# Kernel optimization log

Measured on AMD Instinct MI355X. Metric: run time of the kernel, lower is better.

The kernel has to match this reference:

```python
import jax, jax.numpy as jnp
import numpy as np

B, T, C, H, E, K = 4, 2048, 1024, 2048, 8, 2


def setup_inputs() -> dict:
    key = jax.random.key(0)
    ks = jax.random.split(key, 9)
    s = lambda k, shape, fan: jax.random.normal(k, shape, jnp.float32) / np.sqrt(fan)
    return {
        "x": jax.random.normal(ks[0], (B, T, C), jnp.float32),
        "gate_w": s(ks[1], (C, E), C),            # router gate (no bias)
        "sg_w": s(ks[2], (C, H), C),              # shared expert: gate proj
        "su_w": s(ks[3], (C, H), C),              # shared expert: up proj
        "sd_w": s(ks[4], (H, C), H),              # shared expert: down proj
        "eg_w": s(ks[5], (E, C, H), C),           # routed experts: gate proj
        "eu_w": s(ks[6], (E, C, H), C),           # routed experts: up proj
        "ed_w": s(ks[7], (E, H, C), H),           # routed experts: down proj
    }


def _swiglu(x, wg, wu, wd):
    # x: (B,T,C) -> (B,T,C)
    return jnp.einsum("bth,hc->btc", jax.nn.silu(jnp.einsum("btc,ch->bth", x, wg)) * jnp.einsum("btc,ch->bth", x, wu), wd)


def reference(x, gate_w, sg_w, su_w, sd_w, eg_w, eu_w, ed_w):
    # Router: top-k over expert logits, softmax over selected logits
    logits = jnp.einsum("btc,ce->bte", x, gate_w)            # (B,T,E)
    topk_logits, topk_idx = jax.lax.top_k(logits, K)         # (B,T,K)
    weights = jax.nn.softmax(topk_logits, axis=-1)           # (B,T,K)
    # Dense per-expert combine weight: w_e[b,t,e] = sum_k weights*(idx==e)
    onehot = jax.nn.one_hot(topk_idx, E, dtype=x.dtype)      # (B,T,K,E)
    dense_w = jnp.einsum("btk,btke->bte", weights, onehot)   # (B,T,E)

    shared_out = _swiglu(x, sg_w, su_w, sd_w)

    # Scan over experts (small fixed E), accumulating weighted expert outputs.
    dense_w_e = jnp.moveaxis(dense_w, -1, 0)                 # (E,B,T)

    def step(acc, params):
        wg, wu, wd, w = params
        return acc + w[..., None] * _swiglu(x, wg, wu, wd), None

    expert_out, _ = jax.lax.scan(step, jnp.zeros_like(x), (eg_w, eu_w, ed_w, dense_w_e))
    return shared_out + expert_out, logits
```

## Files before the change

kernel.cpp:

```cpp
#include <hip/hip_runtime.h>
#include <cstdint>
#include <cstddef>

#define NTOK 8192
#define CDIM 1024
#define HDIM 2048
#define NEXP 8
#define NSEG 9
#define MAXTILES 104

typedef __bf16 bf16;
typedef unsigned short u16;
typedef __attribute__((ext_vector_type(8))) __bf16 bf16x8;
typedef __attribute__((ext_vector_type(4))) float f32x4;

__device__ __forceinline__ u16 f2bf(float f) {
  union { u16 u; __bf16 b; } cv;
  cv.b = (__bf16)f;
  return cv.u;
}

__device__ __forceinline__ void gload_lds16(const bf16* g, bf16* l) {
  __builtin_amdgcn_global_load_lds(
      (const __attribute__((address_space(1))) unsigned int*)g,
      (__attribute__((address_space(3))) unsigned int*)l, 16, 0, 0);
}

__global__ __launch_bounds__(64) void init_kernel(int* __restrict__ counts,
                                                  int* __restrict__ fill) {
  if (threadIdx.x < NEXP) {
    counts[threadIdx.x] = 0;
    fill[threadIdx.x] = 0;
  }
}

__global__ __launch_bounds__(256) void cast_x_kernel(
    const float* __restrict__ src, bf16* __restrict__ dst) {
  size_t i = ((size_t)blockIdx.x * 256 + threadIdx.x) * 8;
  float4 a = *(const float4*)(src + i);
  float4 b = *(const float4*)(src + i + 4);
  bf16x8 p;
  p[0] = (bf16)a.x; p[1] = (bf16)a.y; p[2] = (bf16)a.z; p[3] = (bf16)a.w;
  p[4] = (bf16)b.x; p[5] = (bf16)b.y; p[6] = (bf16)b.z; p[7] = (bf16)b.w;
  *(bf16x8*)(dst + i) = p;
}

__global__ __launch_bounds__(256) void router2_kernel(
    const float* __restrict__ x, const float* __restrict__ gw,
    float* __restrict__ logits_out, int* __restrict__ tk_e,
    float* __restrict__ tk_w, int* __restrict__ counts) {
  int wv = threadIdx.x >> 6, l = threadIdx.x & 63;
  int t = blockIdx.x * 4 + wv;
  const float* xr = x + (size_t)t * CDIM;
  float acc[NEXP];
#pragma unroll
  for (int e = 0; e < NEXP; ++e) acc[e] = 0.f;
  for (int c = l; c < CDIM; c += 64) {
    float xv = xr[c];
    const float* g = gw + (size_t)c * NEXP;
    float4 g0 = *(const float4*)(g);
    float4 g1 = *(const float4*)(g + 4);
    acc[0] += xv * g0.x; acc[1] += xv * g0.y; acc[2] += xv * g0.z; acc[3] += xv * g0.w;
    acc[4] += xv * g1.x; acc[5] += xv * g1.y; acc[6] += xv * g1.z; acc[7] += xv * g1.w;
  }
#pragma unroll
  for (int off = 32; off > 0; off >>= 1) {
#pragma unroll
    for (int e = 0; e < NEXP; ++e) acc[e] += __shfl_xor(acc[e], off, 64);
  }
  int e0 = 0; float l0 = acc[0];
#pragma unroll
  for (int e = 1; e < NEXP; ++e) { if (acc[e] > l0) { l0 = acc[e]; e0 = e; } }
  int e1 = -1; float l1 = -3.4e38f;
#pragma unroll
  for (int e = 0; e < NEXP; ++e) { if (e != e0 && acc[e] > l1) { l1 = acc[e]; e1 = e; } }
  float ex = expf(l1 - l0);
  float w0 = 1.f / (1.f + ex), w1 = ex / (1.f + ex);
  if (l < NEXP) logits_out[(size_t)t * NEXP + l] = acc[l];
  if (l == 0) {
    tk_e[2 * t] = e0; tk_e[2 * t + 1] = e1;
    tk_w[2 * t] = w0; tk_w[2 * t + 1] = w1;
    atomicAdd(&counts[e0], 1);
    atomicAdd(&counts[e1], 1);
  }
}

__global__ __launch_bounds__(256) void offsets_kernel(
    const int* __restrict__ counts, int* __restrict__ offs_g,
    int* __restrict__ tile_seg, int* __restrict__ list_tok) {
  __shared__ int off[NSEG], pad[NSEG], cnt[NSEG], ntot;
  int tid = threadIdx.x;
  if (tid == 0) {
    int tot = 0;
    for (int e = 0; e < NSEG; ++e) {
      int c = (e < NEXP) ? counts[e] : NTOK;
      cnt[e] = c; off[e] = tot;
      int p = (c + 255) & ~255;
      pad[e] = p; tot += p;
    }
    ntot = tot;
  }
  __syncthreads();
  if (tid < NSEG) offs_g[tid] = off[tid];
  for (int gt = tid; gt < MAXTILES; gt += 256) {
    int row = gt * 256, seg = -1;
    if (row < ntot) {
      for (int e = 0; e < NSEG; ++e)
        if (row >= off[e] && row < off[e] + pad[e]) { seg = e; break; }
    }
    tile_seg[gt] = seg;
  }
  for (int e = 0; e < NSEG; ++e)
    for (int i = off[e] + cnt[e] + tid; i < off[e] + pad[e]; i += 256)
      list_tok[i] = 0;
}

__global__ __launch_bounds__(256) void scatter_kernel(
    const int* __restrict__ tk_e, const int* __restrict__ offs,
    int* __restrict__ fill, int* __restrict__ list_tok,
    int* __restrict__ inv) {
  int t = blockIdx.x * 256 + threadIdx.x;
  int e0 = tk_e[2 * t], e1 = tk_e[2 * t + 1];
  int p0 = atomicAdd(&fill[e0], 1);
  int i0 = offs[e0] + p0;
  list_tok[i0] = t; inv[2 * t] = i0;
  int p1 = atomicAdd(&fill[e1], 1);
  int i1 = offs[e1] + p1;
  list_tok[i1] = t; inv[2 * t + 1] = i1;
  list_tok[offs[NEXP] + t] = t;
}

__device__ __forceinline__ void transpose_body(const float* __restrict__ src,
                                               u16* __restrict__ dst, int R, int C) {
  __shared__ uint32_t t32[64 * 33];
  const int tid = threadIdx.x;
  const int r0 = blockIdx.y * 64, c0 = blockIdx.x * 64;
  const int rp = tid >> 3;
  const int cg = tid & 7;
  const float* s0 = src + (size_t)(r0 + 2 * rp) * C + c0 + 8 * cg;
  const float* s1 = s0 + C;
  float4 a0 = *(const float4*)(s0);
  float4 a1 = *(const float4*)(s0 + 4);
  float4 b0 = *(const float4*)(s1);
  float4 b1 = *(const float4*)(s1 + 4);
  uint32_t p[8];
  p[0] = f2bf(a0.x) | ((uint32_t)f2bf(b0.x) << 16);
  p[1] = f2bf(a0.y) | ((uint32_t)f2bf(b0.y) << 16);
  p[2] = f2bf(a0.z) | ((uint32_t)f2bf(b0.z) << 16);
  p[3] = f2bf(a0.w) | ((uint32_t)f2bf(b0.w) << 16);
  p[4] = f2bf(a1.x) | ((uint32_t)f2bf(b1.x) << 16);
  p[5] = f2bf(a1.y) | ((uint32_t)f2bf(b1.y) << 16);
  p[6] = f2bf(a1.z) | ((uint32_t)f2bf(b1.z) << 16);
  p[7] = f2bf(a1.w) | ((uint32_t)f2bf(b1.w) << 16);
#pragma unroll
  for (int c = 0; c < 8; ++c) t32[(8 * cg + c) * 33 + rp] = p[c];
  __syncthreads();
  const int oc = tid >> 2, og = tid & 3;
  const uint32_t* rb = &t32[oc * 33 + 8 * og];
  union { uint32_t w[8]; uint4 v[2]; } u;
#pragma unroll
  for (int k = 0; k < 8; ++k) u.w[k] = rb[k];
  u16* d = dst + (size_t)(c0 + oc) * R + r0 + 16 * og;
  *(uint4*)d = u.v[0];
  *(uint4*)(d + 8) = u.v[1];
}

__global__ __launch_bounds__(256) void transpose_cast_kernel(
    const float* __restrict__ src, u16* __restrict__ dst, int R, int C) {
  transpose_body(src, dst, R, C);
}

__global__ __launch_bounds__(256) void transpose_gu_kernel(
    const float* __restrict__ sg, const float* __restrict__ su,
    const float* __restrict__ eg, const float* __restrict__ eu,
    u16* __restrict__ wTg, u16* __restrict__ wTu) {
  const size_t slot = (size_t)HDIM * CDIM;
  int z = blockIdx.z;
  const float* src; u16* dst;
  if (z == 0)       { src = sg;                 dst = wTg + 8 * slot; }
  else if (z == 1)  { src = su;                 dst = wTu + 8 * slot; }
  else if (z < 10)  { src = eg + (z - 2) * slot;  dst = wTg + (z - 2) * slot; }
  else              { src = eu + (z - 10) * slot; dst = wTu + (z - 10) * slot; }
  transpose_body(src, dst, CDIM, HDIM);
}

__global__ __launch_bounds__(256) void transpose_d_kernel(
    const float* __restrict__ sd, const float* __restrict__ ed,
    u16* __restrict__ wTd) {
  const size_t slot = (size_t)HDIM * CDIM;
  int z = blockIdx.z;
  const float* src; u16* dst;
  if (z == 0) { src = sd;                 dst = wTd + 8 * slot; }
  else        { src = ed + (z - 1) * slot; dst = wTd + (z - 1) * slot; }
  transpose_body(src, dst, HDIM, CDIM);
}


#define PHASE_READS_BEGIN __builtin_amdgcn_sched_barrier(0)
#define PHASE_COMPUTE     asm volatile("s_waitcnt lgkmcnt(0)" ::: "memory"); \
                          __builtin_amdgcn_sched_barrier(0);                 \
                          __builtin_amdgcn_s_setprio(1)
#define PHASE_END         __builtin_amdgcn_s_setprio(0)

__global__ __launch_bounds__(512, 2) void gemm_gu5(
    const bf16* __restrict__ xb, const bf16* __restrict__ wTg,
    const bf16* __restrict__ wTu, const int* __restrict__ tile_seg,
    const int* __restrict__ list_tok, bf16* __restrict__ act) {
  __shared__ __align__(16) bf16 sS[2][32768];
  __shared__ int tokLds[256];

  const int nwg = gridDim.x;
  const int bid = blockIdx.x;
  const int wid = (bid & 7) * (nwg >> 3) + (bid >> 3);
  const int tileIdx = wid % MAXTILES;
  const int colIdx = wid / MAXTILES;
  const int seg = tile_seg[tileIdx];
  if (seg < 0) return;

  const int tid = threadIdx.x, l = tid & 63, wv = tid >> 6;
  const int wr = wv >> 2, wn = wv & 3;
  const int n0 = colIdx * 128;
  const size_t rowbase = (size_t)tileIdx * 256;

  if (tid < 256) tokLds[tid] = list_tok[rowbase + tid];
  __syncthreads();

  const int row8 = tid >> 3;
  const int scol = (((tid & 7) ^ (row8 & 7)) << 3);
  const bf16* gA0 = xb + (size_t)tokLds[row8] * CDIM + scol;
  const bf16* gA1 = xb + (size_t)tokLds[64 + row8] * CDIM + scol;
  const bf16* gA2 = xb + (size_t)tokLds[128 + row8] * CDIM + scol;
  const bf16* gA3 = xb + (size_t)tokLds[192 + row8] * CDIM + scol;
  const size_t wslot = (size_t)seg * HDIM * CDIM;
  const bf16* gBg = wTg + wslot + (size_t)(n0 + row8) * CDIM + scol;
  const bf16* gBu = wTu + wslot + (size_t)(n0 + row8) * CDIM + scol;
  const int t8 = tid * 8;

  const int fr = l & 15, kq = l >> 4;
  const int cS0 = ((kq ^ (l & 7)) << 4);
  const int cS1 = (((4 | kq) ^ (l & 7)) << 4);
  const int aBase = (wr * 128 + fr) * 128;
  const int gBase = 32768 + (wn * 32 + fr) * 128;
  const int uBase = 49152 + (wn * 32 + fr) * 128;

  f32x4 accG[2][4][2], accU[2][4][2];
#pragma unroll
  for (int h = 0; h < 2; ++h)
#pragma unroll
    for (int i = 0; i < 4; ++i)
#pragma unroll
      for (int j = 0; j < 2; ++j) {
        accG[h][i][j] = (f32x4){0.f, 0.f, 0.f, 0.f};
        accU[h][i][j] = (f32x4){0.f, 0.f, 0.f, 0.f};
      }

  auto stage_all = [&](int b, int k0) {
    bf16* d = &sS[b][0];
    gload_lds16(gA0 + k0, d + t8);
    gload_lds16(gA1 + k0, d + 4096 + t8);
    gload_lds16(gA2 + k0, d + 8192 + t8);
    gload_lds16(gA3 + k0, d + 12288 + t8);
    gload_lds16(gBg + k0, d + 16384 + t8);
    gload_lds16(gBg + 64 * CDIM + k0, d + 20480 + t8);
    gload_lds16(gBu + k0, d + 24576 + t8);
    gload_lds16(gBu + 64 * CDIM + k0, d + 28672 + t8);
  };

  constexpr int NKT = CDIM / 64;
  stage_all(0, 0);

  for (int kt = 0; kt < NKT; ++kt) {
    const int b = kt & 1, bn = b ^ 1;
    const bool more = (kt + 1 < NKT);
    __builtin_amdgcn_s_barrier();
    if (more) stage_all(bn, (kt + 1) * 64);
    if (more) asm volatile("s_waitcnt vmcnt(8)" ::: "memory");
    else      asm volatile("s_waitcnt vmcnt(0)" ::: "memory");
    __builtin_amdgcn_s_barrier();
    const char* pS = (const char*)&sS[b][0];
    bf16x8 af[4][2], bg[2][2], bu[2][2];

    PHASE_READS_BEGIN;
#pragma unroll
    for (int i = 0; i < 4; ++i) {
      af[i][0] = *(const bf16x8*)(pS + aBase + i * 2048 + cS0);
      af[i][1] = *(const bf16x8*)(pS + aBase + i * 2048 + cS1);
    }
#pragma unroll
    for (int j = 0; j < 2; ++j) {
      bg[j][0] = *(const bf16x8*)(pS + gBase + j * 2048 + cS0);
      bg[j][1] = *(const bf16x8*)(pS + gBase + j * 2048 + cS1);
    }
    PHASE_COMPUTE;
#pragma unroll
    for (int i = 0; i < 4; ++i)
#pragma unroll
      for (int j = 0; j < 2; ++j) {
        accG[0][i][j] = __builtin_amdgcn_mfma_f32_16x16x32_bf16(af[i][0], bg[j][0], accG[0][i][j], 0, 0, 0);
        accG[0][i][j] = __builtin_amdgcn_mfma_f32_16x16x32_bf16(af[i][1], bg[j][1], accG[0][i][j], 0, 0, 0);
      }
    PHASE_END;

    PHASE_READS_BEGIN;
#pragma unroll
    for (int j = 0; j < 2; ++j) {
      bu[j][0] = *(const bf16x8*)(pS + uBase + j * 2048 + cS0);
      bu[j][1] = *(const bf16x8*)(pS + uBase + j * 2048 + cS1);
    }
    PHASE_COMPUTE;
#pragma unroll
    for (int i = 0; i < 4; ++i)
#pragma unroll
      for (int j = 0; j < 2; ++j) {
        accU[0][i][j] = __builtin_amdgcn_mfma_f32_16x16x32_bf16(af[i][0], bu[j][0], accU[0][i][j], 0, 0, 0);
        accU[0][i][j] = __builtin_amdgcn_mfma_f32_16x16x32_bf16(af[i][1], bu[j][1], accU[0][i][j], 0, 0, 0);
      }
    PHASE_END;

    PHASE_READS_BEGIN;
#pragma unroll
    for (int i = 0; i < 4; ++i) {
      af[i][0] = *(const bf16x8*)(pS + aBase + 8192 + i * 2048 + cS0);
      af[i][1] = *(const bf16x8*)(pS + aBase + 8192 + i * 2048 + cS1);
    }
    PHASE_COMPUTE;
#pragma unroll
    for (int i = 0; i < 4; ++i)
#pragma unroll
      for (int j = 0; j < 2; ++j) {
        accG[1][i][j] = __builtin_amdgcn_mfma_f32_16x16x32_bf16(af[i][0], bg[j][0], accG[1][i][j], 0, 0, 0);
        accG[1][i][j] = __builtin_amdgcn_mfma_f32_16x16x32_bf16(af[i][1], bg[j][1], accG[1][i][j], 0, 0, 0);
      }
    PHASE_END;

    __builtin_amdgcn_s_setprio(1);
#pragma unroll
    for (int i = 0; i < 4; ++i)
#pragma unroll
      for (int j = 0; j < 2; ++j) {
        accU[1][i][j] = __builtin_amdgcn_mfma_f32_16x16x32_bf16(af[i][0], bu[j][0], accU[1][i][j], 0, 0, 0);
        accU[1][i][j] = __builtin_amdgcn_mfma_f32_16x16x32_bf16(af[i][1], bu[j][1], accU[1][i][j], 0, 0, 0);
      }
    __builtin_amdgcn_s_setprio(0);
  }

  const int cn = n0 + wn * 32 + fr;
  const int rb = wr * 128 + kq * 4;
#pragma unroll
  for (int h = 0; h < 2; ++h)
#pragma unroll
    for (int i = 0; i < 4; ++i)
#pragma unroll
      for (int r = 0; r < 4; ++r) {
        const size_t row = rowbase + rb + h * 64 + i * 16 + r;
#pragma unroll
        for (int j = 0; j < 2; ++j) {
          float g = accG[h][i][j][r], uu = accU[h][i][j][r];
          float s = g / (1.f + expf(-g));
          act[row * HDIM + cn + j * 16] = (bf16)(s * uu);
        }
      }
}

__global__ __launch_bounds__(512, 2) void gemm_down5(
    const bf16* __restrict__ act, const bf16* __restrict__ wTd,
    const int* __restrict__ tile_seg, bf16* __restrict__ dbuf) {
  __shared__ __align__(16) bf16 sS[2][32768];

  const int nwg = gridDim.x;
  const int bid = blockIdx.x;
  const int wid = (bid & 7) * (nwg >> 3) + (bid >> 3);
  const int tileIdx = wid % MAXTILES;
  const int colIdx = wid / MAXTILES;
  const int seg = tile_seg[tileIdx];
  if (seg < 0) return;

  const int tid = threadIdx.x, l = tid & 63, wv = tid >> 6;
  const int wr = wv >> 2, wn = wv & 3;
  const int n0 = colIdx * 256;
  const size_t rowbase = (size_t)tileIdx * 256;

  const int row8 = tid >> 3;
  const int scol = (((tid & 7) ^ (row8 & 7)) << 3);
  const bf16* gA0 = act + (rowbase + row8) * HDIM + scol;
  const bf16* gA1 = act + (rowbase + 64 + row8) * HDIM + scol;
  const bf16* gA2 = act + (rowbase + 128 + row8) * HDIM + scol;
  const bf16* gA3 = act + (rowbase + 192 + row8) * HDIM + scol;
  const bf16* gB  = wTd + (size_t)seg * CDIM * HDIM + (size_t)(n0 + row8) * HDIM + scol;
  const int t8 = tid * 8;

  const int fr = l & 15, kq = l >> 4;
  const int cS0 = ((kq ^ (l & 7)) << 4);
  const int cS1 = (((4 | kq) ^ (l & 7)) << 4);
  const int aBase = (wr * 128 + fr) * 128;
  const int bBase = 32768 + (wn * 64 + fr) * 128;

  f32x4 acc[2][2][4][2];
#pragma unroll
  for (int h = 0; h < 2; ++h)
#pragma unroll
    for (int nh = 0; nh < 2; ++nh)
#pragma unroll
      for (int i = 0; i < 4; ++i)
#pragma unroll
        for (int j = 0; j < 2; ++j) acc[h][nh][i][j] = (f32x4){0.f, 0.f, 0.f, 0.f};

  auto stage_all = [&](int b, int k0) {
    bf16* d = &sS[b][0];
    gload_lds16(gA0 + k0, d + t8);
    gload_lds16(gA1 + k0, d + 4096 + t8);
    gload_lds16(gA2 + k0, d + 8192 + t8);
    gload_lds16(gA3 + k0, d + 12288 + t8);
    gload_lds16(gB + k0, d + 16384 + t8);
    gload_lds16(gB + 64 * HDIM + k0, d + 20480 + t8);
    gload_lds16(gB + 128 * HDIM + k0, d + 24576 + t8);
    gload_lds16(gB + 192 * HDIM + k0, d + 28672 + t8);
  };

  constexpr int NKT = HDIM / 64;
  stage_all(0, 0);

  for (int kt = 0; kt < NKT; ++kt) {
    const int b = kt & 1, bn = b ^ 1;
    const bool more = (kt + 1 < NKT);
    __builtin_amdgcn_s_barrier();
    if (more) stage_all(bn, (kt + 1) * 64);
    if (more) asm volatile("s_waitcnt vmcnt(8)" ::: "memory");
    else      asm volatile("s_waitcnt vmcnt(0)" ::: "memory");
    __builtin_amdgcn_s_barrier();
    const char* pS = (const char*)&sS[b][0];
    bf16x8 af[4][2], bfr[2][2][2];

    PHASE_READS_BEGIN;
#pragma unroll
    for (int i = 0; i < 4; ++i) {
      af[i][0] = *(const bf16x8*)(pS + aBase + i * 2048 + cS0);
      af[i][1] = *(const bf16x8*)(pS + aBase + i * 2048 + cS1);
    }
#pragma unroll
    for (int j = 0; j < 2; ++j) {
      bfr[0][j][0] = *(const bf16x8*)(pS + bBase + j * 2048 + cS0);
      bfr[0][j][1] = *(const bf16x8*)(pS + bBase + j * 2048 + cS1);
    }
    PHASE_COMPUTE;
#pragma unroll
    for (int i = 0; i < 4; ++i)
#pragma unroll
      for (int j = 0; j < 2; ++j) {
        acc[0][0][i][j] = __builtin_amdgcn_mfma_f32_16x16x32_bf16(af[i][0], bfr[0][j][0], acc[0][0][i][j], 0, 0, 0);
        acc[0][0][i][j] = __builtin_amdgcn_mfma_f32_16x16x32_bf16(af[i][1], bfr[0][j][1], acc[0][0][i][j], 0, 0, 0);
      }
    PHASE_END;

    PHASE_READS_BEGIN;
#pragma unroll
    for (int j = 0; j < 2; ++j) {
      bfr[1][j][0] = *(const bf16x8*)(pS + bBase + 4096 + j * 2048 + cS0);
      bfr[1][j][1] = *(const bf16x8*)(pS + bBase + 4096 + j * 2048 + cS1);
    }
    PHASE_COMPUTE;
#pragma unroll
    for (int i = 0; i < 4; ++i)
#pragma unroll
      for (int j = 0; j < 2; ++j) {
        acc[0][1][i][j] = __builtin_amdgcn_mfma_f32_16x16x32_bf16(af[i][0], bfr[1][j][0], acc[0][1][i][j], 0, 0, 0);
        acc[0][1][i][j] = __builtin_amdgcn_mfma_f32_16x16x32_bf16(af[i][1], bfr[1][j][1], acc[0][1][i][j], 0, 0, 0);
      }
    PHASE_END;

    PHASE_READS_BEGIN;
#pragma unroll
    for (int i = 0; i < 4; ++i) {
      af[i][0] = *(const bf16x8*)(pS + aBase + 8192 + i * 2048 + cS0);
      af[i][1] = *(const bf16x8*)(pS + aBase + 8192 + i * 2048 + cS1);
    }
    PHASE_COMPUTE;
#pragma unroll
    for (int i = 0; i < 4; ++i)
#pragma unroll
      for (int j = 0; j < 2; ++j) {
        acc[1][0][i][j] = __builtin_amdgcn_mfma_f32_16x16x32_bf16(af[i][0], bfr[0][j][0], acc[1][0][i][j], 0, 0, 0);
        acc[1][0][i][j] = __builtin_amdgcn_mfma_f32_16x16x32_bf16(af[i][1], bfr[0][j][1], acc[1][0][i][j], 0, 0, 0);
      }
    PHASE_END;

    __builtin_amdgcn_s_setprio(1);
#pragma unroll
    for (int i = 0; i < 4; ++i)
#pragma unroll
      for (int j = 0; j < 2; ++j) {
        acc[1][1][i][j] = __builtin_amdgcn_mfma_f32_16x16x32_bf16(af[i][0], bfr[1][j][0], acc[1][1][i][j], 0, 0, 0);
        acc[1][1][i][j] = __builtin_amdgcn_mfma_f32_16x16x32_bf16(af[i][1], bfr[1][j][1], acc[1][1][i][j], 0, 0, 0);
      }
    __builtin_amdgcn_s_setprio(0);
  }

  const int rb = wr * 128 + kq * 4;
#pragma unroll
  for (int h = 0; h < 2; ++h)
#pragma unroll
    for (int i = 0; i < 4; ++i)
#pragma unroll
      for (int r = 0; r < 4; ++r) {
        const size_t row = rowbase + rb + h * 64 + i * 16 + r;
#pragma unroll
        for (int nh = 0; nh < 2; ++nh)
#pragma unroll
          for (int j = 0; j < 2; ++j)
            dbuf[row * CDIM + n0 + wn * 64 + nh * 32 + j * 16 + fr] = (bf16)acc[h][nh][i][j][r];
      }
}

__global__ __launch_bounds__(128) void combine_kernel(
    const bf16* __restrict__ dbuf, const int* __restrict__ offs,
    const int* __restrict__ inv, const float* __restrict__ tk_w,
    float* __restrict__ out) {
  const int t = blockIdx.x;
  const int c = threadIdx.x * 8;
  const int rsh = offs[NEXP] + t;
  const int i0 = inv[2 * t], i1 = inv[2 * t + 1];
  const float w0 = tk_w[2 * t], w1 = tk_w[2 * t + 1];
  bf16x8 a = *(const bf16x8*)(dbuf + (size_t)rsh * CDIM + c);
  bf16x8 b = *(const bf16x8*)(dbuf + (size_t)i0 * CDIM + c);
  bf16x8 d = *(const bf16x8*)(dbuf + (size_t)i1 * CDIM + c);
  float* op = out + (size_t)t * CDIM + c;
#pragma unroll
  for (int j = 0; j < 8; ++j)
    op[j] = (float)a[j] + w0 * (float)b[j] + w1 * (float)d[j];
}

__global__ __launch_bounds__(256) void router_kernel(
    const float* __restrict__ x, const float* __restrict__ gw,
    float* __restrict__ dense_w, float* __restrict__ logits_out) {
  int wv = threadIdx.x >> 6, l = threadIdx.x & 63;
  int t = blockIdx.x * 4 + wv;
  const float* xr = x + (size_t)t * CDIM;
  float acc[NEXP];
#pragma unroll
  for (int e = 0; e < NEXP; ++e) acc[e] = 0.f;
  for (int c = l; c < CDIM; c += 64) {
    float xv = xr[c];
    const float* g = gw + (size_t)c * NEXP;
    float4 g0 = *(const float4*)(g);
    float4 g1 = *(const float4*)(g + 4);
    acc[0] += xv * g0.x; acc[1] += xv * g0.y; acc[2] += xv * g0.z; acc[3] += xv * g0.w;
    acc[4] += xv * g1.x; acc[5] += xv * g1.y; acc[6] += xv * g1.z; acc[7] += xv * g1.w;
  }
#pragma unroll
  for (int off = 32; off > 0; off >>= 1) {
#pragma unroll
    for (int e = 0; e < NEXP; ++e) acc[e] += __shfl_xor(acc[e], off, 64);
  }
  int e0 = 0; float l0 = acc[0];
#pragma unroll
  for (int e = 1; e < NEXP; ++e) { if (acc[e] > l0) { l0 = acc[e]; e0 = e; } }
  int e1 = -1; float l1 = -3.4e38f;
#pragma unroll
  for (int e = 0; e < NEXP; ++e) { if (e != e0 && acc[e] > l1) { l1 = acc[e]; e1 = e; } }
  float ex = expf(l1 - l0);
  float w0 = 1.f / (1.f + ex), w1 = ex / (1.f + ex);
  if (l < NEXP) {
    dense_w[(size_t)t * NEXP + l] = (l == e0) ? w0 : ((l == e1) ? w1 : 0.f);
    logits_out[(size_t)t * NEXP + l] = acc[l];
  }
}

template <int MODE>
__global__ __launch_bounds__(256) void gemm_bt(
    const bf16* __restrict__ A, const bf16* __restrict__ Bt,
    int K, int N,
    bf16* __restrict__ Dbf, const bf16* __restrict__ Gin,
    float* __restrict__ outAcc, const float* __restrict__ denseW, int expertId) {
  __shared__ __align__(16) bf16 sA[128 * 32];
  __shared__ __align__(16) bf16 sB[128 * 32];
  const int tid = threadIdx.x;
  const int l = tid & 63, wv = tid >> 6;
  const int wr = wv >> 1, wc = wv & 1;
  const int m0 = blockIdx.y * 128, n0 = blockIdx.x * 128;
  f32x4 acc[4][4];
#pragma unroll
  for (int i = 0; i < 4; ++i)
#pragma unroll
    for (int j = 0; j < 4; ++j) acc[i][j] = (f32x4){0.f, 0.f, 0.f, 0.f};
  const int srow = wv * 16 + (l >> 2);
  const int scol = (l & 3) * 8;
  const bf16* gA = A + (size_t)(m0 + srow) * K + scol;
  const bf16* gB = Bt + (size_t)(n0 + srow) * K + scol;
  bf16* lA = sA + srow * 32 + scol;
  bf16* lB = sB + srow * 32 + scol;
  const int fr = l & 15, fk = (l >> 4) * 8;
  const bf16* rA = sA + (size_t)(wr * 64 + fr) * 32 + fk;
  const bf16* rB = sB + (size_t)(wc * 64 + fr) * 32 + fk;
  for (int k0 = 0; k0 < K; k0 += 32) {
    __syncthreads();
    gload_lds16(gA, lA);
    gload_lds16(gA + (size_t)64 * K, lA + 64 * 32);
    gload_lds16(gB, lB);
    gload_lds16(gB + (size_t)64 * K, lB + 64 * 32);
    gA += 32; gB += 32;
    __syncthreads();
    bf16x8 af[4], bfr[4];
#pragma unroll
    for (int i = 0; i < 4; ++i) af[i] = *(const bf16x8*)(rA + i * 16 * 32);
#pragma unroll
    for (int j = 0; j < 4; ++j) bfr[j] = *(const bf16x8*)(rB + j * 16 * 32);
#pragma unroll
    for (int i = 0; i < 4; ++i)
#pragma unroll
      for (int j = 0; j < 4; ++j)
        acc[i][j] = __builtin_amdgcn_mfma_f32_16x16x32_bf16(af[i], bfr[j], acc[i][j], 0, 0, 0);
  }
  const int cn = n0 + wc * 64 + (l & 15);
  const int rb = m0 + wr * 64 + (l >> 4) * 4;
#pragma unroll
  for (int i = 0; i < 4; ++i)
#pragma unroll
    for (int r = 0; r < 4; ++r) {
      const int m = rb + i * 16 + r;
#pragma unroll
      for (int j = 0; j < 4; ++j) {
        const int n = cn + j * 16;
        float v = acc[i][j][r];
        if (MODE == 0) {
          Dbf[(size_t)m * N + n] = (bf16)v;
        } else if (MODE == 1) {
          float g = (float)Gin[(size_t)m * N + n];
          float s = g / (1.f + expf(-g));
          Dbf[(size_t)m * N + n] = (bf16)(s * v);
        } else if (MODE == 2) {
          outAcc[(size_t)m * N + n] = v;
        } else {
          float w = denseW[(size_t)m * NEXP + expertId];
          outAcc[(size_t)m * N + n] += w * v;
        }
      }
    }
}

extern "C" void kernel_launch(void* const* d_in, const int* in_sizes, int n_in,
                              void* d_out, int out_size, void* d_ws, size_t ws_size,
                              hipStream_t stream) {
  const float* x    = (const float*)d_in[0];
  const float* gate = (const float*)d_in[1];
  const float* sg   = (const float*)d_in[2];
  const float* su   = (const float*)d_in[3];
  const float* sd   = (const float*)d_in[4];
  const float* eg   = (const float*)d_in[5];
  const float* eu   = (const float*)d_in[6];
  const float* ed   = (const float*)d_in[7];
  float* out    = (float*)d_out;
  float* logits = out + (size_t)NTOK * CDIM;

  const size_t MB = 1u << 20;
  const size_t full_need = 226 * MB;

  if (ws_size >= full_need) {
    char* ws = (char*)d_ws;
    bf16*  xb   = (bf16*)(ws);
    bf16*  wTg  = (bf16*)(ws + 16 * MB);
    bf16*  wTu  = (bf16*)(ws + 52 * MB);
    bf16*  act  = (bf16*)(ws + 88 * MB);
    bf16*  wTd  = (bf16*)(ws);
    bf16*  dbuf = (bf16*)(ws + 36 * MB);
    char*  sm   = ws + 200 * MB;
    int*   list_tok = (int*)(sm);
    int*   inv      = (int*)(sm + 128 * 1024);
    int*   tk_e     = (int*)(sm + 256 * 1024);
    float* tk_w     = (float*)(sm + 320 * 1024);
    int*   tile_seg = (int*)(sm + 384 * 1024);
    int*   counts   = (int*)(sm + 388 * 1024);
    int*   fill     = (int*)(sm + 389 * 1024);
    int*   offs     = (int*)(sm + 390 * 1024);

    init_kernel<<<1, 64, 0, stream>>>(counts, fill);
    cast_x_kernel<<<NTOK * CDIM / (256 * 8), 256, 0, stream>>>(x, xb);
    router2_kernel<<<NTOK / 4, 256, 0, stream>>>(x, gate, logits, tk_e, tk_w, counts);
    offsets_kernel<<<1, 256, 0, stream>>>(counts, offs, tile_seg, list_tok);
    scatter_kernel<<<NTOK / 256, 256, 0, stream>>>(tk_e, offs, fill, list_tok, inv);

    dim3 tgu(HDIM / 64, CDIM / 64, 18);
    transpose_gu_kernel<<<tgu, 256, 0, stream>>>(sg, su, eg, eu, (u16*)wTg, (u16*)wTu);

    gemm_gu5<<<(HDIM / 128) * MAXTILES, 512, 0, stream>>>(xb, wTg, wTu, tile_seg, list_tok, act);

    dim3 tdd(CDIM / 64, HDIM / 64, 9);
    transpose_d_kernel<<<tdd, 256, 0, stream>>>(sd, ed, (u16*)wTd);

    gemm_down5<<<(CDIM / 256) * MAXTILES, 512, 0, stream>>>(act, wTd, tile_seg, dbuf);
    combine_kernel<<<NTOK, 128, 0, stream>>>(dbuf, offs, inv, tk_w, out);
    return;
  }

  char* ws = (char*)d_ws;
  bf16*  xb   = (bf16*)(ws);
  bf16*  wTgf = (bf16*)(ws + 16 * MB);
  bf16*  wTuf = (bf16*)(ws + 20 * MB);
  bf16*  wTdf = (bf16*)(ws + 24 * MB);
  bf16*  gbuf = (bf16*)(ws + 28 * MB);
  float* dw   = (float*)(ws + 60 * MB);
  if (ws_size < 60 * MB + (size_t)NTOK * NEXP * sizeof(float)) return;

  cast_x_kernel<<<NTOK * CDIM / (256 * 8), 256, 0, stream>>>(x, xb);
  router_kernel<<<NTOK / 4, 256, 0, stream>>>(x, gate, dw, logits);

  dim3 tg1(HDIM / 64, CDIM / 64);
  dim3 tg2(CDIM / 64, HDIM / 64);
  dim3 g1(HDIM / 128, NTOK / 128);
  dim3 g2(CDIM / 128, NTOK / 128);

  transpose_cast_kernel<<<tg1, 256, 0, stream>>>(sg, (u16*)wTgf, CDIM, HDIM);
  transpose_cast_kernel<<<tg1, 256, 0, stream>>>(su, (u16*)wTuf, CDIM, HDIM);
  transpose_cast_kernel<<<tg2, 256, 0, stream>>>(sd, (u16*)wTdf, HDIM, CDIM);
  gemm_bt<0><<<g1, 256, 0, stream>>>(xb, wTgf, CDIM, HDIM, gbuf, nullptr, nullptr, nullptr, 0);
  gemm_bt<1><<<g1, 256, 0, stream>>>(xb, wTuf, CDIM, HDIM, gbuf, gbuf, nullptr, nullptr, 0);
  gemm_bt<2><<<g2, 256, 0, stream>>>(gbuf, wTdf, HDIM, CDIM, nullptr, nullptr, out, nullptr, 0);

  for (int e = 0; e < NEXP; ++e) {
    const float* egp = eg + (size_t)e * CDIM * HDIM;
    const float* eup = eu + (size_t)e * CDIM * HDIM;
    const float* edp = ed + (size_t)e * HDIM * CDIM;
    transpose_cast_kernel<<<tg1, 256, 0, stream>>>(egp, (u16*)wTgf, CDIM, HDIM);
    transpose_cast_kernel<<<tg1, 256, 0, stream>>>(eup, (u16*)wTuf, CDIM, HDIM);
    transpose_cast_kernel<<<tg2, 256, 0, stream>>>(edp, (u16*)wTdf, HDIM, CDIM);
    gemm_bt<0><<<g1, 256, 0, stream>>>(xb, wTgf, CDIM, HDIM, gbuf, nullptr, nullptr, nullptr, 0);
    gemm_bt<1><<<g1, 256, 0, stream>>>(xb, wTuf, CDIM, HDIM, gbuf, gbuf, nullptr, nullptr, 0);
    gemm_bt<3><<<g2, 256, 0, stream>>>(gbuf, wTdf, HDIM, CDIM, nullptr, nullptr, out, dw, e);
  }
}
```

Measured before the change: 941.7 us.

## Halve GEMM N-tiles, load weight fragments directly to registers, raise occupancy

Both grouped GEMMs (gate/up and down) now stage only the gathered activation tile in LDS. Weight fragments are read straight from global memory into registers in MFMA layout, and the N-tile width is halved. This cuts LDS use from 128KB to 64KB per block so launch bounds can target 4 blocks per CU, with twice as many workgroups launched. The cost is more total weight traffic through global and L2 and uncoalesced-ish per-lane 16-byte weight loads, and the explicit phase scheduling barriers are dropped.

```diff
diff --git a/kernel.cpp b/kernel.cpp
--- a/kernel.cpp
+++ b/kernel.cpp
@@ -196,17 +196,11 @@
 }
 
 
-#define PHASE_READS_BEGIN __builtin_amdgcn_sched_barrier(0)
-#define PHASE_COMPUTE     asm volatile("s_waitcnt lgkmcnt(0)" ::: "memory"); \
-                          __builtin_amdgcn_sched_barrier(0);                 \
-                          __builtin_amdgcn_s_setprio(1)
-#define PHASE_END         __builtin_amdgcn_s_setprio(0)
-
-__global__ __launch_bounds__(512, 2) void gemm_gu5(
+__global__ __launch_bounds__(512, 4) void gemm_gu9(
     const bf16* __restrict__ xb, const bf16* __restrict__ wTg,
     const bf16* __restrict__ wTu, const int* __restrict__ tile_seg,
     const int* __restrict__ list_tok, bf16* __restrict__ act) {
-  __shared__ __align__(16) bf16 sS[2][32768];
+  __shared__ __align__(16) bf16 sA[2][16384];
   __shared__ int tokLds[256];
 
   const int nwg = gridDim.x;
@@ -219,7 +213,7 @@
 
   const int tid = threadIdx.x, l = tid & 63, wv = tid >> 6;
   const int wr = wv >> 2, wn = wv & 3;
-  const int n0 = colIdx * 128;
+  const int n0 = colIdx * 64;
   const size_t rowbase = (size_t)tileIdx * 256;
 
   if (tid < 256) tokLds[tid] = list_tok[rowbase + tid];
@@ -231,120 +225,73 @@
   const bf16* gA1 = xb + (size_t)tokLds[64 + row8] * CDIM + scol;
   const bf16* gA2 = xb + (size_t)tokLds[128 + row8] * CDIM + scol;
   const bf16* gA3 = xb + (size_t)tokLds[192 + row8] * CDIM + scol;
+  const int t8 = tid * 8;
+
+  const int fr = l & 15, kq = l >> 4;
   const size_t wslot = (size_t)seg * HDIM * CDIM;
-  const bf16* gBg = wTg + wslot + (size_t)(n0 + row8) * CDIM + scol;
-  const bf16* gBu = wTu + wslot + (size_t)(n0 + row8) * CDIM + scol;
-  const int t8 = tid * 8;
-
-  const int fr = l & 15, kq = l >> 4;
+  const bf16* gBg = wTg + wslot + (size_t)(n0 + wn * 16 + fr) * CDIM + kq * 8;
+  const bf16* gBu = wTu + wslot + (size_t)(n0 + wn * 16 + fr) * CDIM + kq * 8;
+
   const int cS0 = ((kq ^ (l & 7)) << 4);
   const int cS1 = (((4 | kq) ^ (l & 7)) << 4);
   const int aBase = (wr * 128 + fr) * 128;
-  const int gBase = 32768 + (wn * 32 + fr) * 128;
-  const int uBase = 49152 + (wn * 32 + fr) * 128;
-
-  f32x4 accG[2][4][2], accU[2][4][2];
+
+  f32x4 accG[2][4], accU[2][4];
 #pragma unroll
   for (int h = 0; h < 2; ++h)
 #pragma unroll
-    for (int i = 0; i < 4; ++i)
-#pragma unroll
-      for (int j = 0; j < 2; ++j) {
-        accG[h][i][j] = (f32x4){0.f, 0.f, 0.f, 0.f};
-        accU[h][i][j] = (f32x4){0.f, 0.f, 0.f, 0.f};
-      }
-
-  auto stage_all = [&](int b, int k0) {
-    bf16* d = &sS[b][0];
+    for (int i = 0; i < 4; ++i) {
+      accG[h][i] = (f32x4){0.f, 0.f, 0.f, 0.f};
+      accU[h][i] = (f32x4){0.f, 0.f, 0.f, 0.f};
+    }
+
+  auto stageA = [&](int b, int k0) {
+    bf16* d = &sA[b][0];
     gload_lds16(gA0 + k0, d + t8);
     gload_lds16(gA1 + k0, d + 4096 + t8);
     gload_lds16(gA2 + k0, d + 8192 + t8);
     gload_lds16(gA3 + k0, d + 12288 + t8);
-    gload_lds16(gBg + k0, d + 16384 + t8);
-    gload_lds16(gBg + 64 * CDIM + k0, d + 20480 + t8);
-    gload_lds16(gBu + k0, d + 24576 + t8);
-    gload_lds16(gBu + 64 * CDIM + k0, d + 28672 + t8);
   };
 
   constexpr int NKT = CDIM / 64;
-  stage_all(0, 0);
+  stageA(0, 0);
 
   for (int kt = 0; kt < NKT; ++kt) {
     const int b = kt & 1, bn = b ^ 1;
     const bool more = (kt + 1 < NKT);
+    const int kg = kt * 64;
     __builtin_amdgcn_s_barrier();
-    if (more) stage_all(bn, (kt + 1) * 64);
+    bf16x8 bg[2], bu[2];
+    bg[0] = *(const bf16x8*)(gBg + kg);
+    bg[1] = *(const bf16x8*)(gBg + kg + 32);
+    bu[0] = *(const bf16x8*)(gBu + kg);
+    bu[1] = *(const bf16x8*)(gBu + kg + 32);
+    if (more) stageA(bn, kg + 64);
     if (more) asm volatile("s_waitcnt vmcnt(8)" ::: "memory");
-    else      asm volatile("s_waitcnt vmcnt(0)" ::: "memory");
+    else      asm volatile("s_waitcnt vmcnt(4)" ::: "memory");
     __builtin_amdgcn_s_barrier();
-    const char* pS = (const char*)&sS[b][0];
-    bf16x8 af[4][2], bg[2][2], bu[2][2];
-
-    PHASE_READS_BEGIN;
-#pragma unroll
-    for (int i = 0; i < 4; ++i) {
-      af[i][0] = *(const bf16x8*)(pS + aBase + i * 2048 + cS0);
-      af[i][1] = *(const bf16x8*)(pS + aBase + i * 2048 + cS1);
+    const char* pS = (const char*)&sA[b][0];
+    __builtin_amdgcn_s_setprio(1);
+#pragma unroll
+    for (int h = 0; h < 2; ++h) {
+      bf16x8 af0[4], af1[4];
+#pragma unroll
+      for (int i = 0; i < 4; ++i) {
+        af0[i] = *(const bf16x8*)(pS + aBase + h * 8192 + i * 2048 + cS0);
+        af1[i] = *(const bf16x8*)(pS + aBase + h * 8192 + i * 2048 + cS1);
+      }
+#pragma unroll
+      for (int i = 0; i < 4; ++i) {
+        accG[h][i] = __builtin_amdgcn_mfma_f32_16x16x32_bf16(af0[i], bg[0], accG[h][i], 0, 0, 0);
+        accG[h][i] = __builtin_amdgcn_mfma_f32_16x16x32_bf16(af1[i], bg[1], accG[h][i], 0, 0, 0);
+        accU[h][i] = __builtin_amdgcn_mfma_f32_16x16x32_bf16(af0[i], bu[0], accU[h][i], 0, 0, 0);
+        accU[h][i] = __builtin_amdgcn_mfma_f32_16x16x32_bf16(af1[i], bu[1], accU[h][i], 0, 0, 0);
+      }
     }
-#pragma unroll
-    for (int j = 0; j < 2; ++j) {
-      bg[j][0] = *(const bf16x8*)(pS + gBase + j * 2048 + cS0);
-      bg[j][1] = *(const bf16x8*)(pS + gBase + j * 2048 + cS1);
-    }
-    PHASE_COMPUTE;
-#pragma unroll
-    for (int i = 0; i < 4; ++i)
-#pragma unroll
-      for (int j = 0; j < 2; ++j) {
-        accG[0][i][j] = __builtin_amdgcn_mfma_f32_16x16x32_bf16(af[i][0], bg[j][0], accG[0][i][j], 0, 0, 0);
-        accG[0][i][j] = __builtin_amdgcn_mfma_f32_16x16x32_bf16(af[i][1], bg[j][1], accG[0][i][j], 0, 0, 0);
-      }
-    PHASE_END;
-
-    PHASE_READS_BEGIN;
-#pragma unroll
-    for (int j = 0; j < 2; ++j) {
-      bu[j][0] = *(const bf16x8*)(pS + uBase + j * 2048 + cS0);
-      bu[j][1] = *(const bf16x8*)(pS + uBase + j * 2048 + cS1);
-    }
-    PHASE_COMPUTE;
-#pragma unroll
-    for (int i = 0; i < 4; ++i)
-#pragma unroll
-      for (int j = 0; j < 2; ++j) {
-        accU[0][i][j] = __builtin_amdgcn_mfma_f32_16x16x32_bf16(af[i][0], bu[j][0], accU[0][i][j], 0, 0, 0);
-        accU[0][i][j] = __builtin_amdgcn_mfma_f32_16x16x32_bf16(af[i][1], bu[j][1], accU[0][i][j], 0, 0, 0);
-      }
-    PHASE_END;
-
-    PHASE_READS_BEGIN;
-#pragma unroll
-    for (int i = 0; i < 4; ++i) {
-      af[i][0] = *(const bf16x8*)(pS + aBase + 8192 + i * 2048 + cS0);
-      af[i][1] = *(const bf16x8*)(pS + aBase + 8192 + i * 2048 + cS1);
-    }
-    PHASE_COMPUTE;
-#pragma unroll
-    for (int i = 0; i < 4; ++i)
-#pragma unroll
-      for (int j = 0; j < 2; ++j) {
-        accG[1][i][j] = __builtin_amdgcn_mfma_f32_16x16x32_bf16(af[i][0], bg[j][0], accG[1][i][j], 0, 0, 0);
-        accG[1][i][j] = __builtin_amdgcn_mfma_f32_16x16x32_bf16(af[i][1], bg[j][1], accG[1][i][j], 0, 0, 0);
-      }
-    PHASE_END;
-
-    __builtin_amdgcn_s_setprio(1);
-#pragma unroll
-    for (int i = 0; i < 4; ++i)
-#pragma unroll
-      for (int j = 0; j < 2; ++j) {
-        accU[1][i][j] = __builtin_amdgcn_mfma_f32_16x16x32_bf16(af[i][0], bu[j][0], accU[1][i][j], 0, 0, 0);
-        accU[1][i][j] = __builtin_amdgcn_mfma_f32_16x16x32_bf16(af[i][1], bu[j][1], accU[1][i][j], 0, 0, 0);
-      }
     __builtin_amdgcn_s_setprio(0);
   }
 
-  const int cn = n0 + wn * 32 + fr;
+  const int cn = n0 + wn * 16 + fr;
   const int rb = wr * 128 + kq * 4;
 #pragma unroll
   for (int h = 0; h < 2; ++h)
@@ -353,19 +300,16 @@
 #pragma unroll
       for (int r = 0; r < 4; ++r) {
         const size_t row = rowbase + rb + h * 64 + i * 16 + r;
-#pragma unroll
-        for (int j = 0; j < 2; ++j) {
-          float g = accG[h][i][j][r], uu = accU[h][i][j][r];
-          float s = g / (1.f + expf(-g));
-          act[row * HDIM + cn + j * 16] = (bf16)(s * uu);
-        }
+        float g = accG[h][i][r], uu = accU[h][i][r];
+        float s = g / (1.f + expf(-g));
+        act[row * HDIM + cn] = (bf16)(s * uu);
       }
 }
 
-__global__ __launch_bounds__(512, 2) void gemm_down5(
+__global__ __launch_bounds__(512, 4) void gemm_down8(
     const bf16* __restrict__ act, const bf16* __restrict__ wTd,
     const int* __restrict__ tile_seg, bf16* __restrict__ dbuf) {
-  __shared__ __align__(16) bf16 sS[2][32768];
+  __shared__ __align__(16) bf16 sA[2][16384];
 
   const int nwg = gridDim.x;
   const int bid = blockIdx.x;
@@ -377,7 +321,7 @@
 
   const int tid = threadIdx.x, l = tid & 63, wv = tid >> 6;
   const int wr = wv >> 2, wn = wv & 3;
-  const int n0 = colIdx * 256;
+  const int n0 = colIdx * 128;
   const size_t rowbase = (size_t)tileIdx * 256;
 
   const int row8 = tid >> 3;
@@ -386,115 +330,71 @@
   const bf16* gA1 = act + (rowbase + 64 + row8) * HDIM + scol;
   const bf16* gA2 = act + (rowbase + 128 + row8) * HDIM + scol;
   const bf16* gA3 = act + (rowbase + 192 + row8) * HDIM + scol;
-  const bf16* gB  = wTd + (size_t)seg * CDIM * HDIM + (size_t)(n0 + row8) * HDIM + scol;
   const int t8 = tid * 8;
 
   const int fr = l & 15, kq = l >> 4;
+  const bf16* gB = wTd + (size_t)seg * CDIM * HDIM
+                 + (size_t)(n0 + wn * 32 + fr) * HDIM + kq * 8;
+
   const int cS0 = ((kq ^ (l & 7)) << 4);
   const int cS1 = (((4 | kq) ^ (l & 7)) << 4);
   const int aBase = (wr * 128 + fr) * 128;
-  const int bBase = 32768 + (wn * 64 + fr) * 128;
-
-  f32x4 acc[2][2][4][2];
+
+  f32x4 acc[2][4][2];
 #pragma unroll
   for (int h = 0; h < 2; ++h)
 #pragma unroll
-    for (int nh = 0; nh < 2; ++nh)
-#pragma unroll
-      for (int i = 0; i < 4; ++i)
-#pragma unroll
-        for (int j = 0; j < 2; ++j) acc[h][nh][i][j] = (f32x4){0.f, 0.f, 0.f, 0.f};
-
-  auto stage_all = [&](int b, int k0) {
-    bf16* d = &sS[b][0];
+    for (int i = 0; i < 4; ++i)
+#pragma unroll
+      for (int j = 0; j < 2; ++j) acc[h][i][j] = (f32x4){0.f, 0.f, 0.f, 0.f};
+
+  auto stageA = [&](int b, int k0) {
+    bf16* d = &sA[b][0];
     gload_lds16(gA0 + k0, d + t8);
     gload_lds16(gA1 + k0, d + 4096 + t8);
     gload_lds16(gA2 + k0, d + 8192 + t8);
     gload_lds16(gA3 + k0, d + 12288 + t8);
-    gload_lds16(gB + k0, d + 16384 + t8);
-    gload_lds16(gB + 64 * HDIM + k0, d + 20480 + t8);
-    gload_lds16(gB + 128 * HDIM + k0, d + 24576 + t8);
-    gload_lds16(gB + 192 * HDIM + k0, d + 28672 + t8);
   };
 
   constexpr int NKT = HDIM / 64;
-  stage_all(0, 0);
+  stageA(0, 0);
 
   for (int kt = 0; kt < NKT; ++kt) {
     const int b = kt & 1, bn = b ^ 1;
     const bool more = (kt + 1 < NKT);
+    const int kg = kt * 64;
     __builtin_amdgcn_s_barrier();
-    if (more) stage_all(bn, (kt + 1) * 64);
+    bf16x8 bf0[2], bf1[2];
+    bf0[0] = *(const bf16x8*)(gB + kg);
+    bf0[1] = *(const bf16x8*)(gB + kg + 32);
+    bf1[0] = *(const bf16x8*)(gB + (size_t)16 * HDIM + kg);
+    bf1[1] = *(const bf16x8*)(gB + (size_t)16 * HDIM + kg + 32);
+    if (more) stageA(bn, kg + 64);
     if (more) asm volatile("s_waitcnt vmcnt(8)" ::: "memory");
-    else      asm volatile("s_waitcnt vmcnt(0)" ::: "memory");
+    else      asm volatile("s_waitcnt vmcnt(4)" ::: "memory");
     __builtin_amdgcn_s_barrier();
-    const char* pS = (const char*)&sS[b][0];
-    bf16x8 af[4][2], bfr[2][2][2];
-
-    PHASE_READS_BEGIN;
-#pragma unroll
-    for (int i = 0; i < 4; ++i) {
-      af[i][0] = *(const bf16x8*)(pS + aBase + i * 2048 + cS0);
-      af[i][1] = *(const bf16x8*)(pS + aBase + i * 2048 + cS1);
+    const char* pS = (const char*)&sA[b][0];
+    __builtin_amdgcn_s_setprio(1);
+#pragma unroll
+    for (int h = 0; h < 2; ++h) {
+      bf16x8 af0[4], af1[4];
+#pragma unroll
+      for (int i = 0; i < 4; ++i) {
+        af0[i] = *(const bf16x8*)(pS + aBase + h * 8192 + i * 2048 + cS0);
+        af1[i] = *(const bf16x8*)(pS + aBase + h * 8192 + i * 2048 + cS1);
+      }
+#pragma unroll
+      for (int i = 0; i < 4; ++i) {
+        acc[h][i][0] = __builtin_amdgcn_mfma_f32_16x16x32_bf16(af0[i], bf0[0], acc[h][i][0], 0, 0, 0);
+        acc[h][i][0] = __builtin_amdgcn_mfma_f32_16x16x32_bf16(af1[i], bf0[1], acc[h][i][0], 0, 0, 0);
+        acc[h][i][1] = __builtin_amdgcn_mfma_f32_16x16x32_bf16(af0[i], bf1[0], acc[h][i][1], 0, 0, 0);
+        acc[h][i][1] = __builtin_amdgcn_mfma_f32_16x16x32_bf16(af1[i], bf1[1], acc[h][i][1], 0, 0, 0);
+      }
     }
-#pragma unroll
-    for (int j = 0; j < 2; ++j) {
-      bfr[0][j][0] = *(const bf16x8*)(pS + bBase + j * 2048 + cS0);
-      bfr[0][j][1] = *(const bf16x8*)(pS + bBase + j * 2048 + cS1);
-    }
-    PHASE_COMPUTE;
-#pragma unroll
-    for (int i = 0; i < 4; ++i)
-#pragma unroll
-      for (int j = 0; j < 2; ++j) {
-        acc[0][0][i][j] = __builtin_amdgcn_mfma_f32_16x16x32_bf16(af[i][0], bfr[0][j][0], acc[0][0][i][j], 0, 0, 0);
-        acc[0][0][i][j] = __builtin_amdgcn_mfma_f32_16x16x32_bf16(af[i][1], bfr[0][j][1], acc[0][0][i][j], 0, 0, 0);
-      }
-    PHASE_END;
-
-    PHASE_READS_BEGIN;
-#pragma unroll
-    for (int j = 0; j < 2; ++j) {
-      bfr[1][j][0] = *(const bf16x8*)(pS + bBase + 4096 + j * 2048 + cS0);
-      bfr[1][j][1] = *(const bf16x8*)(pS + bBase + 4096 + j * 2048 + cS1);
-    }
-    PHASE_COMPUTE;
-#pragma unroll
-    for (int i = 0; i < 4; ++i)
-#pragma unroll
-      for (int j = 0; j < 2; ++j) {
-        acc[0][1][i][j] = __builtin_amdgcn_mfma_f32_16x16x32_bf16(af[i][0], bfr[1][j][0], acc[0][1][i][j], 0, 0, 0);
-        acc[0][1][i][j] = __builtin_amdgcn_mfma_f32_16x16x32_bf16(af[i][1], bfr[1][j][1], acc[0][1][i][j], 0, 0, 0);
-      }
-    PHASE_END;
-
-    PHASE_READS_BEGIN;
-#pragma unroll
-    for (int i = 0; i < 4; ++i) {
-      af[i][0] = *(const bf16x8*)(pS + aBase + 8192 + i * 2048 + cS0);
-      af[i][1] = *(const bf16x8*)(pS + aBase + 8192 + i * 2048 + cS1);
-    }
-    PHASE_COMPUTE;
-#pragma unroll
-    for (int i = 0; i < 4; ++i)
-#pragma unroll
-      for (int j = 0; j < 2; ++j) {
-        acc[1][0][i][j] = __builtin_amdgcn_mfma_f32_16x16x32_bf16(af[i][0], bfr[0][j][0], acc[1][0][i][j], 0, 0, 0);
-        acc[1][0][i][j] = __builtin_amdgcn_mfma_f32_16x16x32_bf16(af[i][1], bfr[0][j][1], acc[1][0][i][j], 0, 0, 0);
-      }
-    PHASE_END;
-
-    __builtin_amdgcn_s_setprio(1);
-#pragma unroll
-    for (int i = 0; i < 4; ++i)
-#pragma unroll
-      for (int j = 0; j < 2; ++j) {
-        acc[1][1][i][j] = __builtin_amdgcn_mfma_f32_16x16x32_bf16(af[i][0], bfr[1][j][0], acc[1][1][i][j], 0, 0, 0);
-        acc[1][1][i][j] = __builtin_amdgcn_mfma_f32_16x16x32_bf16(af[i][1], bfr[1][j][1], acc[1][1][i][j], 0, 0, 0);
-      }
     __builtin_amdgcn_s_setprio(0);
   }
 
+  const int cn = n0 + wn * 32 + fr;
   const int rb = wr * 128 + kq * 4;
 #pragma unroll
   for (int h = 0; h < 2; ++h)
@@ -504,10 +404,8 @@
       for (int r = 0; r < 4; ++r) {
         const size_t row = rowbase + rb + h * 64 + i * 16 + r;
 #pragma unroll
-        for (int nh = 0; nh < 2; ++nh)
-#pragma unroll
-          for (int j = 0; j < 2; ++j)
-            dbuf[row * CDIM + n0 + wn * 64 + nh * 32 + j * 16 + fr] = (bf16)acc[h][nh][i][j][r];
+        for (int j = 0; j < 2; ++j)
+          dbuf[row * CDIM + cn + j * 16] = (bf16)acc[h][i][j][r];
       }
 }
 
@@ -681,12 +579,12 @@
     dim3 tgu(HDIM / 64, CDIM / 64, 18);
     transpose_gu_kernel<<<tgu, 256, 0, stream>>>(sg, su, eg, eu, (u16*)wTg, (u16*)wTu);
 
-    gemm_gu5<<<(HDIM / 128) * MAXTILES, 512, 0, stream>>>(xb, wTg, wTu, tile_seg, list_tok, act);
+    gemm_gu9<<<(HDIM / 64) * MAXTILES, 512, 0, stream>>>(xb, wTg, wTu, tile_seg, list_tok, act);
 
     dim3 tdd(CDIM / 64, HDIM / 64, 9);
     transpose_d_kernel<<<tdd, 256, 0, stream>>>(sd, ed, (u16*)wTd);
 
-    gemm_down5<<<(CDIM / 256) * MAXTILES, 512, 0, stream>>>(act, wTd, tile_seg, dbuf);
+    gemm_down8<<<(CDIM / 128) * MAXTILES, 512, 0, stream>>>(act, wTd, tile_seg, dbuf);
     combine_kernel<<<NTOK, 128, 0, stream>>>(dbuf, offs, inv, tk_w, out);
     return;
   }
```

New measurement: 1.045 ms. 1.11x slower.
